# Performance work log

Measured on AMD Instinct MI355X. Metric: run time of the kernel, lower is better.

Reference implementation:

```python
import jax, jax.numpy as jnp
import numpy as np

B, T, C = 2, 4096, 768
H = 12
D = C // H  # head_size = 64


def setup_inputs() -> dict:
    key = jax.random.key(0)
    k1, k2, k3 = jax.random.split(key, 3)
    x = jax.random.normal(k1, (B, T, C), dtype=jnp.float32)
    w_attn = jax.random.normal(k2, (C, 3 * C), dtype=jnp.float32) * (C ** -0.5)
    b_attn = jnp.zeros((3 * C,), dtype=jnp.float32)
    w_proj = jax.random.normal(k3, (C, C), dtype=jnp.float32) * (C ** -0.5)
    b_proj = jnp.zeros((C,), dtype=jnp.float32)
    return {"x": x, "w_attn": w_attn, "b_attn": b_attn, "w_proj": w_proj, "b_proj": b_proj}


def reference(x, w_attn, b_attn, w_proj, b_proj):
    Bx, Tx, Cx = x.shape
    # fused QKV projection
    qkv = x @ w_attn + b_attn  # (B, T, 3C)
    q, k, v = jnp.split(qkv, 3, axis=2)
    # (B, H, T, D)
    q = q.reshape(Bx, Tx, H, D).transpose(0, 2, 1, 3)
    k = k.reshape(Bx, Tx, H, D).transpose(0, 2, 1, 3)
    v = v.reshape(Bx, Tx, H, D).transpose(0, 2, 1, 3)
    scale = 1.0 / jnp.sqrt(jnp.asarray(D, dtype=x.dtype))
    scores = jnp.einsum('bhqd,bhkd->bhqk', q, k) * scale  # (B, H, T, T)
    causal = jnp.tril(jnp.ones((Tx, Tx), dtype=bool))
    scores = jnp.where(causal, scores, jnp.asarray(-jnp.inf, dtype=scores.dtype))
    attn = jax.nn.softmax(scores, axis=-1)
    y = jnp.einsum('bhqk,bhkd->bhqd', attn, v)  # (B, H, T, D)
    y = y.transpose(0, 2, 1, 3).reshape(Bx, Tx, Cx)
    return y @ w_proj + b_proj
```

## Files before the change

kernel.cpp:

```cpp
#include <hip/hip_runtime.h>
#include <stdint.h>

#define B_   2
#define T_   4096
#define C_   768
#define H_   12
#define D_   64
#define BH_  24
#define M_   8192
#define K_   768
#define N1_  2304

#define NEG_BIG (-1.0e30f)
#define QSCALE 0.18033688011112042f

typedef short bf16x8 __attribute__((ext_vector_type(8)));
typedef float f32x4  __attribute__((ext_vector_type(4)));
typedef float f32x16 __attribute__((ext_vector_type(16)));
typedef uint32_t u32x4 __attribute__((ext_vector_type(4)));
typedef int i32x2 __attribute__((ext_vector_type(2)));

typedef const __attribute__((address_space(1))) void* as1cv;
typedef __attribute__((address_space(3))) void*       as3v;

__device__ __forceinline__ void gload_lds16(const void* g, void* l) {
  __builtin_amdgcn_global_load_lds((as1cv)g, (as3v)l, 16, 0, 0);
}

__device__ __forceinline__ unsigned short f2bf(float f) {
  uint32_t x = __builtin_bit_cast(uint32_t, f);
  uint32_t r = (x + 0x7fffu + ((x >> 16) & 1u)) >> 16;
  return (unsigned short)r;
}

__device__ __forceinline__ unsigned short f2bf_hu(float f) {
  return (unsigned short)((__builtin_bit_cast(uint32_t, f) + 0x8000u) >> 16);
}

#if __has_builtin(__builtin_amdgcn_perm)
__device__ __forceinline__ uint32_t pack_hu(float lo, float hi) {
  uint32_t a = __builtin_bit_cast(uint32_t, lo) + 0x8000u;
  uint32_t b = __builtin_bit_cast(uint32_t, hi) + 0x8000u;
  return __builtin_amdgcn_perm(b, a, 0x07060302u);
}
#else
__device__ __forceinline__ uint32_t pack_hu(float lo, float hi) {
  uint32_t a = __builtin_bit_cast(uint32_t, lo) + 0x8000u;
  uint32_t b = __builtin_bit_cast(uint32_t, hi) + 0x8000u;
  return (b & 0xFFFF0000u) | (a >> 16);
}
#endif

__device__ __forceinline__ float bfu(uint32_t w, int hb) {
  return __builtin_bit_cast(float, hb ? (w & 0xFFFF0000u) : (w << 16));
}

#if __has_builtin(__builtin_amdgcn_permlane32_swap)
#define HAVE_PLSWAP 1
#else
#define HAVE_PLSWAP 0
#endif

#if __has_builtin(__builtin_amdgcn_exp2f)
__device__ __forceinline__ float fast_exp2(float x) { return __builtin_amdgcn_exp2f(x); }
#else
__device__ __forceinline__ float fast_exp2(float x) { return __expf(x * 0.69314718056f); }
#endif

__global__ void cast_kernel(const float* __restrict__ in, unsigned short* __restrict__ out, int n4) {
  int idx = blockIdx.x * blockDim.x + threadIdx.x;
  int stride = gridDim.x * blockDim.x;
  for (int i = idx; i < n4; i += stride) {
    float4 v = reinterpret_cast<const float4*>(in)[i];
    ushort4 o;
    o.x = f2bf(v.x); o.y = f2bf(v.y); o.z = f2bf(v.z); o.w = f2bf(v.w);
    reinterpret_cast<ushort4*>(out)[i] = o;
  }
}

__global__ void transpose_cast2(const float* __restrict__ a, unsigned short* __restrict__ oa,
                                const float* __restrict__ b, unsigned short* __restrict__ ob) {
  __shared__ float tile[32][33];
  const int bx = blockIdx.x;
  const float* in; unsigned short* out; int N, cb;
  if (bx < 72) { in = a; out = oa; N = 2304; cb = bx; }
  else         { in = b; out = ob; N = 768;  cb = bx - 72; }
  const int tx = threadIdx.x, ty = threadIdx.y;
  const int n = cb * 32 + tx;
  #pragma unroll
  for (int r = 0; r < 4; ++r) {
    int k = blockIdx.y * 32 + ty + r * 8;
    tile[ty + r * 8][tx] = in[(size_t)k * N + n];
  }
  __syncthreads();
  const int k = blockIdx.y * 32 + tx;
  #pragma unroll
  for (int r = 0; r < 4; ++r) {
    int nn = cb * 32 + ty + r * 8;
    out[(size_t)nn * K_ + k] = f2bf(tile[tx][ty + r * 8]);
  }
}

template <int MODE>
__global__ __launch_bounds__(256) void gemm_kernel(
    const unsigned short* __restrict__ A, const unsigned short* __restrict__ BT,
    const float* __restrict__ bias,
    unsigned short* __restrict__ o0, unsigned short* __restrict__ o1,
    unsigned short* __restrict__ o2, float* __restrict__ fo) {
  __shared__ __align__(16) unsigned short Al[128 * 32];
  __shared__ __align__(16) unsigned short Bl[128 * 32];
  const int tid = threadIdx.x;
  const int w = tid >> 6, lane = tid & 63;
  const int g = lane >> 4, c16 = lane & 15;
  const int wr = w >> 1, wc = w & 1;
  const int m0 = blockIdx.x * 128, n0 = blockIdx.y * 128;

  f32x4 acc[4][4] = {};

  for (int k0 = 0; k0 < K_; k0 += 32) {
    __syncthreads();
    #pragma unroll
    for (int q = 0; q < 2; ++q) {
      const int ch = (w * 2 + q) * 64 + lane;
      const int row = ch >> 2, kb = ch & 3;
      gload_lds16(A  + (size_t)(m0 + row) * K_ + k0 + kb * 8, &Al[(w * 2 + q) * 512]);
      gload_lds16(BT + (size_t)(n0 + row) * K_ + k0 + kb * 8, &Bl[(w * 2 + q) * 512]);
    }
    __syncthreads();
    bf16x8 af[4], bfr[4];
    #pragma unroll
    for (int i = 0; i < 4; ++i) {
      af[i]  = *reinterpret_cast<const bf16x8*>(&Al[(wr * 64 + i * 16 + c16) * 32 + g * 8]);
      bfr[i] = *reinterpret_cast<const bf16x8*>(&Bl[(wc * 64 + i * 16 + c16) * 32 + g * 8]);
    }
    #pragma unroll
    for (int i = 0; i < 4; ++i)
      #pragma unroll
      for (int j = 0; j < 4; ++j)
        acc[i][j] = __builtin_amdgcn_mfma_f32_16x16x32_bf16(af[i], bfr[j], acc[i][j], 0, 0, 0);
  }

  const int which = (MODE == 0) ? (n0 / 768) : 0;
  #pragma unroll
  for (int i = 0; i < 4; ++i) {
    const int mbase = m0 + wr * 64 + i * 16 + g * 4;
    const int bb2 = mbase >> 12, tb = mbase & 4095;
    #pragma unroll
    for (int j2 = 0; j2 < 4; ++j2) {
      const int n = n0 + wc * 64 + j2 * 16 + c16;
      const float bv = bias[n];
      if constexpr (MODE == 0) {
        const int cc = n - which * 768;
        const int hh2 = cc >> 6, dd = cc & 63;
        const size_t hb = ((size_t)bb2 * H_ + hh2) * T_ * D_;
        if (which == 0) {
          const int addr0 = tb * 64 + dd;
          #pragma unroll
          for (int j = 0; j < 4; ++j)
            o0[hb + addr0 + j * 64] = f2bf_hu((acc[i][j2][j] + bv) * QSCALE);
        } else if (which == 1) {
          const int addr0 = ((tb >> 5) * 4 + (dd >> 4)) * 512 +
                            ((tb & 31) + ((dd >> 3) & 1) * 32) * 8 + (dd & 7);
          #pragma unroll
          for (int j = 0; j < 4; ++j)
            o1[hb + addr0 + j * 8] = f2bf_hu(acc[i][j2][j] + bv);
        } else {
          const int addr0 = (tb >> 6) * 4096 + (dd >> 5) * 2048 +
                            ((tb >> 4) & 3) * 512 +
                            ((dd & 31) + ((tb >> 3) & 1) * 32) * 8 + (tb & 7);
          #pragma unroll
          for (int j = 0; j < 4; ++j)
            o2[hb + addr0 + j] = f2bf_hu(acc[i][j2][j] + bv);
        }
      } else {
        #pragma unroll
        for (int j = 0; j < 4; ++j)
          fo[(size_t)(mbase + j) * 768 + n] = acc[i][j2][j] + bv;
      }
    }
  }
}

__global__ __launch_bounds__(256, 2) void attn_kernel(
    const unsigned short* __restrict__ Qb, const unsigned short* __restrict__ Kb,
    const unsigned short* __restrict__ Vt, unsigned short* __restrict__ Yb) {
  __shared__ float Ml[3][2][64];
  __shared__ float Ll[3][2][64];
  __shared__ uint32_t Ylp[3][32][64];

  const int tidx = threadIdx.x;
  const int wv = tidx >> 6;
  const int lane = tidx & 63;
  const int q31 = lane & 31, hi = lane >> 5;
  const int bid = blockIdx.x;
  const int bh = bid % BH_;
  const int strip = (T_ / 64 - 1) - bid / BH_;
  const int q0 = strip * 64;
  const int qgA = q0 + q31;
  const int qgB = q0 + 32 + q31;

  const int bb = bh / H_, hh = bh % H_;
  const size_t hoff = (size_t)bh * T_ * D_;
  const unsigned short* Qh = Qb + hoff;
  const unsigned short* Kh = Kb + hoff + lane * 8;
  const unsigned short* Vh = Vt + hoff + lane * 8;

  bf16x8 qfA[4], qfB[4];
  #pragma unroll
  for (int s = 0; s < 4; ++s) {
    qfA[s] = *reinterpret_cast<const bf16x8*>(&Qh[(size_t)qgA * D_ + s * 16 + hi * 8]);
    qfB[s] = *reinterpret_cast<const bf16x8*>(&Qh[(size_t)qgB * D_ + s * 16 + hi * 8]);
  }

  float mA = NEG_BIG, lA = 0.f, mB = NEG_BIG, lB = 0.f;
  f32x16 yA0 = {}, yA1 = {}, yB0 = {}, yB1 = {};

  const int nt = strip + 1;

  bf16x8 kf[8];
  {
    const unsigned short* kT = Kh + wv * 4096;
    #pragma unroll
    for (int s = 0; s < 8; ++s)
      kf[s] = *reinterpret_cast<const bf16x8*>(kT + (s >> 2) * 2048 + (s & 3) * 512);
  }

  for (int it = wv; it < nt; it += 4) {
    const int kv0 = it << 6;

    const unsigned short* vT = Vh + it * 4096;
    bf16x8 vlo[4], vhi[4];
    #pragma unroll
    for (int ks = 0; ks < 4; ++ks) {
      vlo[ks] = *reinterpret_cast<const bf16x8*>(vT + ks * 512);
      vhi[ks] = *reinterpret_cast<const bf16x8*>(vT + 2048 + ks * 512);
    }

    f32x16 sA0 = {}, sA1 = {}, sB0 = {}, sB1 = {};
    #pragma unroll
    for (int s = 0; s < 4; ++s) {
      sA0 = __builtin_amdgcn_mfma_f32_32x32x16_bf16(kf[s], qfA[s], sA0, 0, 0, 0);
      sB0 = __builtin_amdgcn_mfma_f32_32x32x16_bf16(kf[s], qfB[s], sB0, 0, 0, 0);
    }
    #pragma unroll
    for (int s = 0; s < 4; ++s) {
      sA1 = __builtin_amdgcn_mfma_f32_32x32x16_bf16(kf[4 + s], qfA[s], sA1, 0, 0, 0);
      sB1 = __builtin_amdgcn_mfma_f32_32x32x16_bf16(kf[4 + s], qfB[s], sB1, 0, 0, 0);
    }

    {
      const unsigned short* kT = Kh + (it + 4) * 4096;
      #pragma unroll
      for (int s = 0; s < 8; ++s)
        kf[s] = *reinterpret_cast<const bf16x8*>(kT + (s >> 2) * 2048 + (s & 3) * 512);
    }

    if (it == strip) {
      #pragma unroll
      for (int r = 0; r < 16; ++r) {
        const int kvl = (r & 3) + 8 * (r >> 2) + 4 * hi;
        sA0[r] = (kv0 + kvl > qgA)      ? NEG_BIG : sA0[r];
        sA1[r] = NEG_BIG;
        sB1[r] = (kv0 + 32 + kvl > qgB) ? NEG_BIG : sB1[r];
      }
    }

    {
      float a[16];
      #pragma unroll
      for (int r = 0; r < 8; ++r) a[r] = fmaxf(sA0[2 * r], sA0[2 * r + 1]);
      #pragma unroll
      for (int r = 0; r < 8; ++r) a[8 + r] = fmaxf(sA1[2 * r], sA1[2 * r + 1]);
      #pragma unroll
      for (int st = 8; st > 0; st >>= 1)
        #pragma unroll
        for (int r = 0; r < 16; ++r) if (r < st) a[r] = fmaxf(a[r], a[r + st]);
      float tmax = a[0];
      tmax = fmaxf(tmax, __shfl_xor(tmax, 32));

      if (__any(tmax > mA + 11.5f)) {
        const float mnew = fmaxf(mA, tmax);
        const float alpha = fast_exp2(mA - mnew);
        mA = mnew;
        lA *= alpha;
        #pragma unroll
        for (int r = 0; r < 16; ++r) { yA0[r] *= alpha; yA1[r] *= alpha; }
      }
      #pragma unroll
      for (int r = 0; r < 16; ++r) {
        sA0[r] = fast_exp2(sA0[r] - mA);
        sA1[r] = fast_exp2(sA1[r] - mA);
      }
      #pragma unroll
      for (int r = 0; r < 8; ++r) a[r] = sA0[2 * r] + sA0[2 * r + 1];
      #pragma unroll
      for (int r = 0; r < 8; ++r) a[8 + r] = sA1[2 * r] + sA1[2 * r + 1];
      #pragma unroll
      for (int st = 8; st > 0; st >>= 1)
        #pragma unroll
        for (int r = 0; r < 16; ++r) if (r < st) a[r] = a[r] + a[r + st];
      float rsum = a[0];
      rsum += __shfl_xor(rsum, 32);
      lA += rsum;

      bf16x8 pf[4];
#if HAVE_PLSWAP
#define MK_PF(KS, SH, GA, HA)                                                 \
      {                                                                       \
        uint32_t g0 = pack_hu(SH[(GA)*4 + 0], SH[(GA)*4 + 1]);                \
        uint32_t g1 = pack_hu(SH[(GA)*4 + 2], SH[(GA)*4 + 3]);                \
        uint32_t h0 = pack_hu(SH[(HA)*4 + 0], SH[(HA)*4 + 1]);                \
        uint32_t h1 = pack_hu(SH[(HA)*4 + 2], SH[(HA)*4 + 3]);                \
        i32x2 r0 = __builtin_amdgcn_permlane32_swap((int)g0, (int)h0, false, false); \
        i32x2 r1 = __builtin_amdgcn_permlane32_swap((int)g1, (int)h1, false, false); \
        u32x4 t;                                                              \
        t[0] = (uint32_t)r0[0];                                               \
        t[1] = (uint32_t)r1[0];                                               \
        t[2] = (uint32_t)r0[1];                                               \
        t[3] = (uint32_t)r1[1];                                               \
        pf[KS] = __builtin_bit_cast(bf16x8, t);                               \
      }
#else
#define MK_PF(KS, SH, GA, HA)                                                 \
      {                                                                       \
        uint32_t g0 = pack_hu(SH[(GA)*4 + 0], SH[(GA)*4 + 1]);                \
        uint32_t g1 = pack_hu(SH[(GA)*4 + 2], SH[(GA)*4 + 3]);                \
        uint32_t h0 = pack_hu(SH[(HA)*4 + 0], SH[(HA)*4 + 1]);                \
        uint32_t h1 = pack_hu(SH[(HA)*4 + 2], SH[(HA)*4 + 3]);                \
        uint32_t sg0 = (uint32_t)__shfl_xor((int)g0, 32);                     \
        uint32_t sg1 = (uint32_t)__shfl_xor((int)g1, 32);                     \
        uint32_t sh0 = (uint32_t)__shfl_xor((int)h0, 32);                     \
        uint32_t sh1 = (uint32_t)__shfl_xor((int)h1, 32);                     \
        u32x4 t;                                                              \
        t[0] = hi ? sh0 : g0;                                                 \
        t[1] = hi ? sh1 : g1;                                                 \
        t[2] = hi ? h0 : sg0;                                                 \
        t[3] = hi ? h1 : sg1;                                                 \
        pf[KS] = __builtin_bit_cast(bf16x8, t);                               \
      }
#endif
      MK_PF(0, sA0, 0, 1)
      MK_PF(1, sA0, 2, 3)
      MK_PF(2, sA1, 0, 1)
      MK_PF(3, sA1, 2, 3)

      #pragma unroll
      for (int ks = 0; ks < 4; ++ks)
        yA0 = __builtin_amdgcn_mfma_f32_32x32x16_bf16(vlo[ks], pf[ks], yA0, 0, 0, 0);
      #pragma unroll
      for (int ks = 0; ks < 4; ++ks)
        yA1 = __builtin_amdgcn_mfma_f32_32x32x16_bf16(vhi[ks], pf[ks], yA1, 0, 0, 0);
    }

    {
      float a[16];
      #pragma unroll
      for (int r = 0; r < 8; ++r) a[r] = fmaxf(sB0[2 * r], sB0[2 * r + 1]);
      #pragma unroll
      for (int r = 0; r < 8; ++r) a[8 + r] = fmaxf(sB1[2 * r], sB1[2 * r + 1]);
      #pragma unroll
      for (int st = 8; st > 0; st >>= 1)
        #pragma unroll
        for (int r = 0; r < 16; ++r) if (r < st) a[r] = fmaxf(a[r], a[r + st]);
      float tmax = a[0];
      tmax = fmaxf(tmax, __shfl_xor(tmax, 32));

      if (__any(tmax > mB + 11.5f)) {
        const float mnew = fmaxf(mB, tmax);
        const float alpha = fast_exp2(mB - mnew);
        mB = mnew;
        lB *= alpha;
        #pragma unroll
        for (int r = 0; r < 16; ++r) { yB0[r] *= alpha; yB1[r] *= alpha; }
      }
      #pragma unroll
      for (int r = 0; r < 16; ++r) {
        sB0[r] = fast_exp2(sB0[r] - mB);
        sB1[r] = fast_exp2(sB1[r] - mB);
      }
      #pragma unroll
      for (int r = 0; r < 8; ++r) a[r] = sB0[2 * r] + sB0[2 * r + 1];
      #pragma unroll
      for (int r = 0; r < 8; ++r) a[8 + r] = sB1[2 * r] + sB1[2 * r + 1];
      #pragma unroll
      for (int st = 8; st > 0; st >>= 1)
        #pragma unroll
        for (int r = 0; r < 16; ++r) if (r < st) a[r] = a[r] + a[r + st];
      float rsum = a[0];
      rsum += __shfl_xor(rsum, 32);
      lB += rsum;

      bf16x8 pf[4];
      MK_PF(0, sB0, 0, 1)
      MK_PF(1, sB0, 2, 3)
      MK_PF(2, sB1, 0, 1)
      MK_PF(3, sB1, 2, 3)
#undef MK_PF

      #pragma unroll
      for (int ks = 0; ks < 4; ++ks)
        yB0 = __builtin_amdgcn_mfma_f32_32x32x16_bf16(vlo[ks], pf[ks], yB0, 0, 0, 0);
      #pragma unroll
      for (int ks = 0; ks < 4; ++ks)
        yB1 = __builtin_amdgcn_mfma_f32_32x32x16_bf16(vhi[ks], pf[ks], yB1, 0, 0, 0);
    }
  }

  if (wv > 0) {
    Ml[wv - 1][0][lane] = mA; Ml[wv - 1][1][lane] = mB;
    Ll[wv - 1][0][lane] = lA; Ll[wv - 1][1][lane] = lB;
    #pragma unroll
    for (int r = 0; r < 8; ++r) {
      Ylp[wv - 1][r][lane]      = pack_hu(yA0[2 * r], yA0[2 * r + 1]);
      Ylp[wv - 1][8 + r][lane]  = pack_hu(yA1[2 * r], yA1[2 * r + 1]);
      Ylp[wv - 1][16 + r][lane] = pack_hu(yB0[2 * r], yB0[2 * r + 1]);
      Ylp[wv - 1][24 + r][lane] = pack_hu(yB1[2 * r], yB1[2 * r + 1]);
    }
  }
  __syncthreads();
  if (wv == 0) {
    {
      float mm = mA;
      #pragma unroll
      for (int p = 0; p < 3; ++p) mm = fmaxf(mm, Ml[p][0][lane]);
      const float aw = fast_exp2(mA - mm);
      float ap[3];
      float ll = lA * aw;
      #pragma unroll
      for (int p = 0; p < 3; ++p) {
        ap[p] = fast_exp2(Ml[p][0][lane] - mm);
        ll += Ll[p][0][lane] * ap[p];
      }
      const float inv = 1.f / ll;
      const size_t ro = ((size_t)bb * T_ + qgA) * C_ + hh * D_;
      #pragma unroll
      for (int q2 = 0; q2 < 4; ++q2) {
        float v[8];
        #pragma unroll
        for (int e = 0; e < 4; ++e) {
          const int pr = q2 * 2 + (e >> 1), hb2 = e & 1;
          float t0 = yA0[q2 * 4 + e] * aw;
          float t1 = yA1[q2 * 4 + e] * aw;
          #pragma unroll
          for (int p = 0; p < 3; ++p) {
            t0 += bfu(Ylp[p][pr][lane], hb2) * ap[p];
            t1 += bfu(Ylp[p][8 + pr][lane], hb2) * ap[p];
          }
          v[e] = t0 * inv;
          v[4 + e] = t1 * inv;
        }
        uint2 pr0 = {pack_hu(v[0], v[1]), pack_hu(v[2], v[3])};
        *reinterpret_cast<uint2*>(&Yb[ro + q2 * 8 + hi * 4]) = pr0;
        uint2 pr1 = {pack_hu(v[4], v[5]), pack_hu(v[6], v[7])};
        *reinterpret_cast<uint2*>(&Yb[ro + 32 + q2 * 8 + hi * 4]) = pr1;
      }
    }
    {
      float mm = mB;
      #pragma unroll
      for (int p = 0; p < 3; ++p) mm = fmaxf(mm, Ml[p][1][lane]);
      const float aw = fast_exp2(mB - mm);
      float ap[3];
      float ll = lB * aw;
      #pragma unroll
      for (int p = 0; p < 3; ++p) {
        ap[p] = fast_exp2(Ml[p][1][lane] - mm);
        ll += Ll[p][1][lane] * ap[p];
      }
      const float inv = 1.f / ll;
      const size_t ro = ((size_t)bb * T_ + qgB) * C_ + hh * D_;
      #pragma unroll
      for (int q2 = 0; q2 < 4; ++q2) {
        float v[8];
        #pragma unroll
        for (int e = 0; e < 4; ++e) {
          const int pr = q2 * 2 + (e >> 1), hb2 = e & 1;
          float t0 = yB0[q2 * 4 + e] * aw;
          float t1 = yB1[q2 * 4 + e] * aw;
          #pragma unroll
          for (int p = 0; p < 3; ++p) {
            t0 += bfu(Ylp[p][16 + pr][lane], hb2) * ap[p];
            t1 += bfu(Ylp[p][24 + pr][lane], hb2) * ap[p];
          }
          v[e] = t0 * inv;
          v[4 + e] = t1 * inv;
        }
        uint2 pr0 = {pack_hu(v[0], v[1]), pack_hu(v[2], v[3])};
        *reinterpret_cast<uint2*>(&Yb[ro + q2 * 8 + hi * 4]) = pr0;
        uint2 pr1 = {pack_hu(v[4], v[5]), pack_hu(v[6], v[7])};
        *reinterpret_cast<uint2*>(&Yb[ro + 32 + q2 * 8 + hi * 4]) = pr1;
      }
    }
  }
}

extern "C" void kernel_launch(void* const* d_in, const int* in_sizes, int n_in,
                              void* d_out, int out_size, void* d_ws, size_t ws_size,
                              hipStream_t stream) {
  const float* x      = (const float*)d_in[0];
  const float* w_attn = (const float*)d_in[1];
  const float* b_attn = (const float*)d_in[2];
  const float* w_proj = (const float*)d_in[3];
  const float* b_proj = (const float*)d_in[4];
  float* out = (float*)d_out;

  char* ws = (char*)d_ws;
  size_t off = 0;
  auto alloc = [&](size_t bytes) -> void* {
    void* p = ws + off;
    off += (bytes + 255) & ~(size_t)255;
    return p;
  };
  unsigned short* xb  = (unsigned short*)alloc((size_t)M_ * K_ * 2);
  unsigned short* waT = (unsigned short*)alloc((size_t)N1_ * K_ * 2);
  unsigned short* wpT = (unsigned short*)alloc((size_t)C_ * K_ * 2);
  unsigned short* Qb  = (unsigned short*)alloc((size_t)BH_ * T_ * D_ * 2);
  unsigned short* Kb  = (unsigned short*)alloc((size_t)BH_ * T_ * D_ * 2);
  unsigned short* Vt  = (unsigned short*)alloc((size_t)BH_ * D_ * T_ * 2);
  unsigned short* Yb  = (unsigned short*)alloc((size_t)M_ * C_ * 2);

  cast_kernel<<<1024, 256, 0, stream>>>(x, xb, M_ * K_ / 4);
  transpose_cast2<<<dim3(96, 24), dim3(32, 8), 0, stream>>>(w_attn, waT, w_proj, wpT);

  gemm_kernel<0><<<dim3(M_ / 128, N1_ / 128), 256, 0, stream>>>(
      xb, waT, b_attn, Qb, Kb, Vt, nullptr);

  attn_kernel<<<(T_ / 64) * BH_, 256, 0, stream>>>(Qb, Kb, Vt, Yb);

  gemm_kernel<1><<<dim3(M_ / 128, C_ / 128), 256, 0, stream>>>(
      Yb, wpT, b_proj, nullptr, nullptr, nullptr, out);
}
```

Measured before the change: 166.7 us.

## Double-buffer GEMM LDS tiles, swizzle workgroup order, use max3 in softmax

Result: no change. 167.5 us (+0.5%).

```diff
diff --git a/kernel.cpp b/kernel.cpp
--- a/kernel.cpp
+++ b/kernel.cpp
@@ -53,6 +53,10 @@
 
 __device__ __forceinline__ float bfu(uint32_t w, int hb) {
   return __builtin_bit_cast(float, hb ? (w & 0xFFFF0000u) : (w << 16));
+}
+
+__device__ __forceinline__ float max3f(float a, float b, float c) {
+  return fmaxf(fmaxf(a, b), c);
 }
 
 #if __has_builtin(__builtin_amdgcn_permlane32_swap)
@@ -107,37 +111,53 @@
     const float* __restrict__ bias,
     unsigned short* __restrict__ o0, unsigned short* __restrict__ o1,
     unsigned short* __restrict__ o2, float* __restrict__ fo) {
-  __shared__ __align__(16) unsigned short Al[128 * 32];
-  __shared__ __align__(16) unsigned short Bl[128 * 32];
+  __shared__ __align__(16) unsigned short Al[2][128 * 32];
+  __shared__ __align__(16) unsigned short Bl[2][128 * 32];
   const int tid = threadIdx.x;
   const int w = tid >> 6, lane = tid & 63;
   const int g = lane >> 4, c16 = lane & 15;
   const int wr = w >> 1, wc = w & 1;
-  const int m0 = blockIdx.x * 128, n0 = blockIdx.y * 128;
-
-  f32x4 acc[4][4] = {};
-
-  for (int k0 = 0; k0 < K_; k0 += 32) {
-    __syncthreads();
+
+  const int gX = gridDim.x;
+  const int nwg = gX * gridDim.y;
+  int lin = blockIdx.y * gX + blockIdx.x;
+  lin = (lin & 7) * (nwg >> 3) + (lin >> 3);
+  const int m0 = (lin % gX) * 128, n0 = (lin / gX) * 128;
+
+  const int NT = K_ / 32;
+
+  auto stage = [&](int t, int buf) {
+    const int k0 = t * 32;
     #pragma unroll
     for (int q = 0; q < 2; ++q) {
       const int ch = (w * 2 + q) * 64 + lane;
       const int row = ch >> 2, kb = ch & 3;
-      gload_lds16(A  + (size_t)(m0 + row) * K_ + k0 + kb * 8, &Al[(w * 2 + q) * 512]);
-      gload_lds16(BT + (size_t)(n0 + row) * K_ + k0 + kb * 8, &Bl[(w * 2 + q) * 512]);
-    }
-    __syncthreads();
+      gload_lds16(A  + (size_t)(m0 + row) * K_ + k0 + kb * 8, &Al[buf][(w * 2 + q) * 512]);
+      gload_lds16(BT + (size_t)(n0 + row) * K_ + k0 + kb * 8, &Bl[buf][(w * 2 + q) * 512]);
+    }
+  };
+
+  f32x4 acc[4][4] = {};
+
+  stage(0, 0);
+  __syncthreads();
+
+  int cur = 0;
+  for (int t = 0; t < NT; ++t) {
+    if (t + 1 < NT) stage(t + 1, cur ^ 1);
     bf16x8 af[4], bfr[4];
     #pragma unroll
     for (int i = 0; i < 4; ++i) {
-      af[i]  = *reinterpret_cast<const bf16x8*>(&Al[(wr * 64 + i * 16 + c16) * 32 + g * 8]);
-      bfr[i] = *reinterpret_cast<const bf16x8*>(&Bl[(wc * 64 + i * 16 + c16) * 32 + g * 8]);
+      af[i]  = *reinterpret_cast<const bf16x8*>(&Al[cur][(wr * 64 + i * 16 + c16) * 32 + g * 8]);
+      bfr[i] = *reinterpret_cast<const bf16x8*>(&Bl[cur][(wc * 64 + i * 16 + c16) * 32 + g * 8]);
     }
     #pragma unroll
     for (int i = 0; i < 4; ++i)
       #pragma unroll
       for (int j = 0; j < 4; ++j)
         acc[i][j] = __builtin_amdgcn_mfma_f32_16x16x32_bf16(af[i], bfr[j], acc[i][j], 0, 0, 0);
+    __syncthreads();
+    cur ^= 1;
   }
 
   const int which = (MODE == 0) ? (n0 / 768) : 0;
@@ -265,18 +285,30 @@
       }
     }
 
+#define COLMAX(S0, S1, TM)                                                    \
+    {                                                                         \
+      float g0 = max3f(S0[0], S0[1], S0[2]);                                  \
+      float g1 = max3f(S0[3], S0[4], S0[5]);                                  \
+      float g2 = max3f(S0[6], S0[7], S0[8]);                                  \
+      float g3 = max3f(S0[9], S0[10], S0[11]);                                \
+      float g4 = max3f(S0[12], S0[13], S0[14]);                               \
+      float g5 = max3f(S0[15], S1[0], S1[1]);                                 \
+      float g6 = max3f(S1[2], S1[3], S1[4]);                                  \
+      float g7 = max3f(S1[5], S1[6], S1[7]);                                  \
+      float g8 = max3f(S1[8], S1[9], S1[10]);                                 \
+      float g9 = max3f(S1[11], S1[12], S1[13]);                               \
+      float ga = fmaxf(S1[14], S1[15]);                                       \
+      float h0 = max3f(g0, g1, g2);                                           \
+      float h1 = max3f(g3, g4, g5);                                           \
+      float h2 = max3f(g6, g7, g8);                                           \
+      float h3 = max3f(g9, ga, h0);                                           \
+      TM = max3f(h1, h2, h3);                                                 \
+      TM = fmaxf(TM, __shfl_xor(TM, 32));                                     \
+    }
+
     {
-      float a[16];
-      #pragma unroll
-      for (int r = 0; r < 8; ++r) a[r] = fmaxf(sA0[2 * r], sA0[2 * r + 1]);
-      #pragma unroll
-      for (int r = 0; r < 8; ++r) a[8 + r] = fmaxf(sA1[2 * r], sA1[2 * r + 1]);
-      #pragma unroll
-      for (int st = 8; st > 0; st >>= 1)
-        #pragma unroll
-        for (int r = 0; r < 16; ++r) if (r < st) a[r] = fmaxf(a[r], a[r + st]);
-      float tmax = a[0];
-      tmax = fmaxf(tmax, __shfl_xor(tmax, 32));
+      float tmax;
+      COLMAX(sA0, sA1, tmax)
 
       if (__any(tmax > mA + 11.5f)) {
         const float mnew = fmaxf(mA, tmax);
@@ -291,6 +323,7 @@
         sA0[r] = fast_exp2(sA0[r] - mA);
         sA1[r] = fast_exp2(sA1[r] - mA);
       }
+      float a[16];
       #pragma unroll
       for (int r = 0; r < 8; ++r) a[r] = sA0[2 * r] + sA0[2 * r + 1];
       #pragma unroll
@@ -353,17 +386,8 @@
     }
 
     {
-      float a[16];
-      #pragma unroll
-      for (int r = 0; r < 8; ++r) a[r] = fmaxf(sB0[2 * r], sB0[2 * r + 1]);
-      #pragma unroll
-      for (int r = 0; r < 8; ++r) a[8 + r] = fmaxf(sB1[2 * r], sB1[2 * r + 1]);
-      #pragma unroll
-      for (int st = 8; st > 0; st >>= 1)
-        #pragma unroll
-        for (int r = 0; r < 16; ++r) if (r < st) a[r] = fmaxf(a[r], a[r + st]);
-      float tmax = a[0];
-      tmax = fmaxf(tmax, __shfl_xor(tmax, 32));
+      float tmax;
+      COLMAX(sB0, sB1, tmax)
 
       if (__any(tmax > mB + 11.5f)) {
         const float mnew = fmaxf(mB, tmax);
@@ -378,6 +402,7 @@
         sB0[r] = fast_exp2(sB0[r] - mB);
         sB1[r] = fast_exp2(sB1[r] - mB);
       }
+      float a[16];
       #pragma unroll
       for (int r = 0; r < 8; ++r) a[r] = sB0[2 * r] + sB0[2 * r + 1];
       #pragma unroll
@@ -396,6 +421,7 @@
       MK_PF(2, sB1, 0, 1)
       MK_PF(3, sB1, 2, 3)
 #undef MK_PF
+#undef COLMAX
 
       #pragma unroll
       for (int ks = 0; ks < 4; ++ks)
```
